# Optimization experiments

Measured on AMD Instinct MI355X. Metric: run time of the kernel, lower is better.

Reference implementation:

```python
import jax, jax.numpy as jnp
import numpy as np

D_MODEL = 1024
N_HEADS = 16
D_HEAD = D_MODEL // N_HEADS
D_FF = 4096
B, L = 4, 2048


def setup_inputs() -> dict:
    key = jax.random.key(0)
    ks = jax.random.split(key, 12)
    s = 0.02
    return {
        "x": jax.random.normal(ks[0], (B, L, D_MODEL), dtype=jnp.float32),
        "ln1_g": jnp.ones((D_MODEL,), jnp.float32),
        "ln1_b": jnp.zeros((D_MODEL,), jnp.float32),
        "w_qkv": jax.random.normal(ks[1], (D_MODEL, 3 * D_MODEL), jnp.float32) * s,
        "b_qkv": jnp.zeros((3 * D_MODEL,), jnp.float32),
        "w_out": jax.random.normal(ks[2], (D_MODEL, D_MODEL), jnp.float32) * s,
        "b_out": jnp.zeros((D_MODEL,), jnp.float32),
        "ln2_g": jnp.ones((D_MODEL,), jnp.float32),
        "ln2_b": jnp.zeros((D_MODEL,), jnp.float32),
        "w1": jax.random.normal(ks[3], (D_MODEL, D_FF), jnp.float32) * s,
        "b1": jnp.zeros((D_FF,), jnp.float32),
        "w2": jax.random.normal(ks[4], (D_FF, D_MODEL), jnp.float32) * s,
        "b2": jnp.zeros((D_MODEL,), jnp.float32),
    }


def _layernorm(x, g, b, eps=1e-5):
    mu = jnp.mean(x, axis=-1, keepdims=True)
    var = jnp.var(x, axis=-1, keepdims=True)
    return (x - mu) * jax.lax.rsqrt(var + eps) * g + b


def _attention(h, w_qkv, b_qkv, w_out, b_out):
    Bx, Lx, D = h.shape
    qkv = h @ w_qkv + b_qkv  # [B,L,3D]
    qkv = qkv.reshape(Bx, Lx, 3, N_HEADS, D_HEAD)
    q, k, v = qkv[:, :, 0], qkv[:, :, 1], qkv[:, :, 2]  # [B,L,H,Dh]
    att = jnp.einsum("bqhd,bkhd->bhqk", q, k) * (D_HEAD ** -0.5)
    causal = jnp.tril(jnp.ones((Lx, Lx), bool))
    att = jnp.where(causal, att, -jnp.inf)
    att = jax.nn.softmax(att, axis=-1)
    out = jnp.einsum("bhqk,bkhd->bqhd", att, v).reshape(Bx, Lx, D)
    return out @ w_out + b_out


def reference(x, ln1_g, ln1_b, w_qkv, b_qkv, w_out, b_out,
              ln2_g, ln2_b, w1, b1, w2, b2):
    h = x + _attention(_layernorm(x, ln1_g, ln1_b), w_qkv, b_qkv, w_out, b_out)
    ff = jax.nn.gelu(_layernorm(h, ln2_g, ln2_b) @ w1 + b1, approximate=False) @ w2 + b2
    return h + ff
```

## Files before the change

### kernel.cpp

```cpp
#include <hip/hip_runtime.h>
#include <hip/hip_bf16.h>


typedef float f32x4 __attribute__((ext_vector_type(4)));
typedef __bf16 bf16x8 __attribute__((ext_vector_type(8)));
typedef unsigned short u16;

#define MFMA16(a, b, c) __builtin_amdgcn_mfma_f32_16x16x32_bf16((a), (b), (c), 0, 0, 0)

#define GLL16(g, l)                                                            \
  __builtin_amdgcn_global_load_lds(                                            \
      (__attribute__((address_space(1))) void*)(g),                            \
      (__attribute__((address_space(3))) void*)(l), 16, 0, 0)

__device__ __forceinline__ u16 f2bf(float f) {
  union { float f; unsigned int u; } x; x.f = f;
  unsigned int r = x.u + 0x7fffu + ((x.u >> 16) & 1u);
  return (u16)(r >> 16);
}

__global__ __launch_bounds__(256) void ln_kernel(
    const float* __restrict__ x, const float* __restrict__ g,
    const float* __restrict__ b, u16* __restrict__ y)
{
  int row = blockIdx.x;
  int t = threadIdx.x;
  const float4* xr = (const float4*)(x + (size_t)row * 1024);
  float4 v = xr[t];
  float s  = v.x + v.y + v.z + v.w;
  float ss = v.x*v.x + v.y*v.y + v.z*v.z + v.w*v.w;
#pragma unroll
  for (int off = 1; off < 64; off <<= 1) {
    s  += __shfl_xor(s, off);
    ss += __shfl_xor(ss, off);
  }
  __shared__ float red[8];
  int w = t >> 6;
  if ((t & 63) == 0) { red[w*2] = s; red[w*2+1] = ss; }
  __syncthreads();
  s  = red[0] + red[2] + red[4] + red[6];
  ss = red[1] + red[3] + red[5] + red[7];
  float mu  = s * (1.0f / 1024.0f);
  float var = ss * (1.0f / 1024.0f) - mu * mu;
  float rs  = rsqrtf(var + 1e-5f);
  float4 gg = ((const float4*)g)[t];
  float4 bb = ((const float4*)b)[t];
  ushort4 o;
  o.x = f2bf((v.x - mu) * rs * gg.x + bb.x);
  o.y = f2bf((v.y - mu) * rs * gg.y + bb.y);
  o.z = f2bf((v.z - mu) * rs * gg.z + bb.z);
  o.w = f2bf((v.w - mu) * rs * gg.w + bb.w);
  ((ushort4*)y)[(size_t)row * 256 + t] = o;
}

__global__ __launch_bounds__(256) void wt_kernel(
    const float* __restrict__ W, u16* __restrict__ Wt, int K, int N)
{
  __shared__ u16 tile[32][33];
  int n0 = blockIdx.x * 32, k0 = blockIdx.y * 32;
  int t = threadIdx.x, tr = t >> 5, tc = t & 31;
#pragma unroll
  for (int i = 0; i < 4; ++i) {
    int k = k0 + tr + i * 8;
    tile[tc][tr + i * 8] = f2bf(W[(size_t)k * N + n0 + tc]);
  }
  __syncthreads();
#pragma unroll
  for (int i = 0; i < 4; ++i) {
    int n = n0 + tr + i * 8;
    Wt[(size_t)n * K + k0 + tc] = tile[tr + i * 8][tc];
  }
}

__global__ __launch_bounds__(256) void vt_kernel(
    const u16* __restrict__ qkv, u16* __restrict__ vt)
{
  __shared__ u16 tile[64][65];
  int bid = blockIdx.x;
  int lt = bid & 31, h = (bid >> 5) & 15, b = bid >> 9;
  int t = threadIdx.x;
  int tr = t >> 4, tc4 = (t & 15) * 4;
  const u16* src = qkv + ((size_t)(b * 2048 + lt * 64)) * 3072 + 2048 + h * 64;
#pragma unroll
  for (int i = 0; i < 4; ++i) {
    int ll = tr + i * 16;
    ushort4 v = *(const ushort4*)(src + (size_t)ll * 3072 + tc4);
    tile[ll][tc4] = v.x; tile[ll][tc4+1] = v.y; tile[ll][tc4+2] = v.z; tile[ll][tc4+3] = v.w;
  }
  __syncthreads();
  u16* dst = vt + ((size_t)(b * 16 + h) * 64) * 2048 + lt * 64;
#pragma unroll
  for (int i = 0; i < 4; ++i) {
    int d = tr + i * 16;
    ushort4 o;
    o.x = tile[tc4][d]; o.y = tile[tc4+1][d]; o.z = tile[tc4+2][d]; o.w = tile[tc4+3][d];
    *(ushort4*)(dst + (size_t)d * 2048 + tc4) = o;
  }
}

template<int BN, int GELU, int HAS_RES, int OUT_BF16>
__global__ __launch_bounds__(512, 2) void gemm_kernel(
    const u16* __restrict__ A, const u16* __restrict__ Bt,
    const float* __restrict__ bias, const float* __restrict__ res,
    void* __restrict__ Cout, int M, int N, int K)
{
  constexpr int WGN = BN / 64;
  constexpr int MW  = (WGN == 4) ? 8 : 4;
  constexpr int LPT = (BN == 256) ? 4 : 3;
  __shared__ u16 lA[4][256 * 32];
  __shared__ u16 lB[4][BN * 32];

  const int nbn = N / BN;
  int nwg = gridDim.x;
  int wg = blockIdx.x;
  if ((nwg & 7) == 0) wg = (wg & 7) * (nwg >> 3) + (wg >> 3);
  int bm = wg / nbn, bn = wg % nbn;
  int tid = threadIdx.x;
  int w = tid >> 6, l = tid & 63;
  int lh = l & 15, lg = l >> 4;
  int wr = w / WGN, wc = w % WGN;
  const size_t Kb = (size_t)K * 2;
  const char* Ab = (const char*)A + (size_t)(bm * 256) * Kb;
  const char* Bb = (const char*)Bt + (size_t)(bn * BN) * Kb;

  const int swst = ((tid ^ (tid >> 3)) & 3) << 4;
  const size_t stR0 = (size_t)(tid >> 2) * Kb + swst;
  const size_t stR1 = stR0 + 128 * Kb;

#define GSTAGE(sel, kt)                                                        \
  do {                                                                         \
    GLL16(Ab + stR0 + (size_t)(kt) * 64, (char*)lA[sel] + tid * 16);           \
    GLL16(Ab + stR1 + (size_t)(kt) * 64, (char*)lA[sel] + tid * 16 + 8192);    \
    GLL16(Bb + stR0 + (size_t)(kt) * 64, (char*)lB[sel] + tid * 16);           \
    if (BN == 256)                                                             \
      GLL16(Bb + stR1 + (size_t)(kt) * 64, (char*)lB[sel] + tid * 16 + 8192);  \
  } while (0)

  const int swo = ((lg ^ (lh >> 1)) & 3) << 4;
  const int offA = (wr * (MW * 16) + lh) * 64 + swo;
  const int offB = (wc * 64 + lh) * 64 + swo;

  f32x4 acc[MW][4] = {};
  const int nkt = K >> 5;
  GSTAGE(0, 0);
  GSTAGE(1, 1);
  GSTAGE(2, 2);
  if (BN == 256) asm volatile("s_waitcnt vmcnt(8)" ::: "memory");
  else           asm volatile("s_waitcnt vmcnt(6)" ::: "memory");
  __builtin_amdgcn_s_barrier();
  __builtin_amdgcn_sched_barrier(0);

#pragma unroll 1
  for (int t = 0; t < nkt; ++t) {
    const char* bufA = (const char*)lA[t & 3];
    const char* bufB = (const char*)lB[t & 3];
    bf16x8 af[MW], bfr[4];
#pragma unroll
    for (int m = 0; m < MW; ++m)
      af[m] = *(const bf16x8*)(bufA + offA + m * 1024);
#pragma unroll
    for (int n = 0; n < 4; ++n)
      bfr[n] = *(const bf16x8*)(bufB + offB + n * 1024);
    if (t + 3 < nkt) GSTAGE((t + 3) & 3, t + 3);
    __builtin_amdgcn_s_setprio(1);
#pragma unroll
    for (int m = 0; m < MW; ++m)
#pragma unroll
      for (int n = 0; n < 4; ++n)
        acc[m][n] = MFMA16(af[m], bfr[n], acc[m][n]);
    __builtin_amdgcn_s_setprio(0);
    if (t < nkt - 1) {
      __builtin_amdgcn_sched_barrier(0);
      if (t < nkt - 3) {
        if (BN == 256) asm volatile("s_waitcnt vmcnt(8)" ::: "memory");
        else           asm volatile("s_waitcnt vmcnt(6)" ::: "memory");
      } else if (t == nkt - 3) {
        if (BN == 256) asm volatile("s_waitcnt vmcnt(4)" ::: "memory");
        else           asm volatile("s_waitcnt vmcnt(3)" ::: "memory");
      } else {
        asm volatile("s_waitcnt vmcnt(0)" ::: "memory");
      }
      __builtin_amdgcn_s_barrier();
      __builtin_amdgcn_sched_barrier(0);
    }
  }
#undef GSTAGE

#pragma unroll
  for (int m = 0; m < MW; ++m) {
    int row0 = bm * 256 + wr * (MW * 16) + m * 16 + lg * 4;
#pragma unroll
    for (int n = 0; n < 4; ++n) {
      int col = bn * BN + wc * 64 + n * 16 + lh;
      float bv = bias[col];
#pragma unroll
      for (int r = 0; r < 4; ++r) {
        int row = row0 + r;
        float v = acc[m][n][r] + bv;
        if (GELU) v = 0.5f * v * (1.0f + erff(v * 0.70710678118f));
        if (HAS_RES) v += res[(size_t)row * N + col];
        if (OUT_BF16) ((u16*)Cout)[(size_t)row * N + col] = f2bf(v);
        else ((float*)Cout)[(size_t)row * N + col] = v;
      }
    }
  }
  (void)M;
}

__global__ __launch_bounds__(256, 4) void attn_kernel(
    const u16* __restrict__ qkv, const u16* __restrict__ vt,
    u16* __restrict__ out)
{
  __shared__ u16 Ks[2][4096];
  __shared__ u16 Vs[2][4096];
  __shared__ u16 Ps[4][1024];

  const float C = 0.18033688011f;

  int bid = blockIdx.x;
  int pi = bid >> 6, bh = bid & 63;
  int b = bh >> 4, h = bh & 15;
  int tid = threadIdx.x;
  int w = tid >> 6, l = tid & 63;
  int lh = l & 15, lg = l >> 4;
  int lh7 = lh & 7;

  const char* kg = (const char*)qkv + (size_t)(b * 2048) * 6144 + 2048 + h * 128;
  const char* vg = (const char*)vt + (size_t)((b * 16 + h) * 64) * 4096;
  char* pbw = (char*)Ps[w] + lh * 128;

#pragma unroll 1
  for (int half = 0; half < 2; ++half) {
    int qb = half ? (31 - pi) : pi;
    int q0 = qb * 64 + w * 16;
    const u16* qbase = qkv + ((size_t)(b * 2048) + q0) * 3072 + h * 64;
    bf16x8 aq0 = *(const bf16x8*)(qbase + (size_t)lh * 3072 + lg * 8);
    bf16x8 aq1 = *(const bf16x8*)(qbase + (size_t)lh * 3072 + 32 + lg * 8);

    f32x4 o[4] = {};
    float m = -1e30f;
    float lsum = 0.f;
    int nt = qb + 1;

    __syncthreads();
#pragma unroll
    for (int i = 0; i < 2; ++i) {
      int u = tid + i * 256;
      int row = u >> 3, uc = u & 7, sw = uc ^ (row & 7);
      GLL16(kg + (size_t)row * 6144 + sw * 16,
            (char*)Ks[0] + (size_t)(i * 256 + w * 64) * 16);
      GLL16(vg + (size_t)row * 4096 + sw * 16,
            (char*)Vs[0] + (size_t)(i * 256 + w * 64) * 16);
    }

#pragma unroll 1
    for (int kt = 0; kt < nt; ++kt) {
      int cur = kt & 1;
      __syncthreads();
      if (kt + 1 < nt) {
        int nxt = cur ^ 1;
        size_t kofs = (size_t)(kt + 1) * 64;
#pragma unroll
        for (int i = 0; i < 2; ++i) {
          int u = tid + i * 256;
          int row = u >> 3, uc = u & 7, sw = uc ^ (row & 7);
          GLL16(kg + (kofs + row) * 6144 + sw * 16,
                (char*)Ks[nxt] + (size_t)(i * 256 + w * 64) * 16);
          GLL16(vg + (size_t)row * 4096 + kofs * 2 + sw * 16,
                (char*)Vs[nxt] + (size_t)(i * 256 + w * 64) * 16);
        }
      }
      const char* kbuf = (const char*)Ks[cur];
      f32x4 s[4];
#pragma unroll
      for (int kb = 0; kb < 4; ++kb) {
        int row = kb * 16 + lh;
        const char* rp = kbuf + row * 128;
        bf16x8 a0 = *(const bf16x8*)(rp + ((lg ^ lh7) << 4));
        bf16x8 a1 = *(const bf16x8*)(rp + (((4 + lg) ^ lh7) << 4));
        f32x4 z = {0.f, 0.f, 0.f, 0.f};
        z = MFMA16(a0, aq0, z);
        z = MFMA16(a1, aq1, z);
        s[kb] = z;
      }
      if (kt == qb) {
        int qin = w * 16 + lh;
#pragma unroll
        for (int kb = 0; kb < 4; ++kb)
#pragma unroll
          for (int r = 0; r < 4; ++r)
            if (kb * 16 + lg * 4 + r > qin) s[kb][r] = -1e30f;
      }
      float tm = fmaxf(fmaxf(s[0][0], s[0][1]), fmaxf(s[0][2], s[0][3]));
#pragma unroll
      for (int kb = 1; kb < 4; ++kb)
        tm = fmaxf(tm, fmaxf(fmaxf(s[kb][0], s[kb][1]), fmaxf(s[kb][2], s[kb][3])));
      tm = fmaxf(tm, __shfl_xor(tm, 16));
      tm = fmaxf(tm, __shfl_xor(tm, 32));
      if (__any(tm > m + 64.0f)) {
        float nm = fmaxf(m, tm);
        float f = __builtin_amdgcn_exp2f((m - nm) * C);
        m = nm; lsum *= f;
#pragma unroll
        for (int db = 0; db < 4; ++db)
#pragma unroll
          for (int r = 0; r < 4; ++r) o[db][r] *= f;
      }
      float mc = m * C;
      float ps = 0.f;
#pragma unroll
      for (int kb = 0; kb < 4; ++kb)
#pragma unroll
        for (int r = 0; r < 4; ++r) {
          float p = __builtin_amdgcn_exp2f(fmaf(s[kb][r], C, -mc));
          s[kb][r] = p;
          ps += p;
        }
      ps += __shfl_xor(ps, 16);
      ps += __shfl_xor(ps, 32);
      lsum += ps;
#pragma unroll
      for (int kb = 0; kb < 4; ++kb) {
        unsigned lo, hi;
        asm("v_cvt_pk_bf16_f32 %0, %1, %2" : "=v"(lo) : "v"(s[kb][0]), "v"(s[kb][1]));
        asm("v_cvt_pk_bf16_f32 %0, %1, %2" : "=v"(hi) : "v"(s[kb][2]), "v"(s[kb][3]));
        int unit = kb * 2 + (lg >> 1);
        uint2 val; val.x = lo; val.y = hi;
        *(uint2*)(pbw + ((unit ^ lh7) << 4) + ((lg & 1) << 3)) = val;
      }
      bf16x8 pa0 = *(const bf16x8*)(pbw + ((lg ^ lh7) << 4));
      bf16x8 pa1 = *(const bf16x8*)(pbw + (((4 + lg) ^ lh7) << 4));
      const char* vbuf = (const char*)Vs[cur];
#pragma unroll
      for (int db = 0; db < 4; ++db) {
        int row = db * 16 + lh;
        const char* rp = vbuf + row * 128;
        bf16x8 v0 = *(const bf16x8*)(rp + ((lg ^ lh7) << 4));
        bf16x8 v1 = *(const bf16x8*)(rp + (((4 + lg) ^ lh7) << 4));
        o[db] = MFMA16(v0, pa0, o[db]);
        o[db] = MFMA16(v1, pa1, o[db]);
      }
    }
    float rinv = 1.0f / lsum;
    u16* ob = out + ((size_t)(b * 2048) + q0 + lh) * 1024 + h * 64;
#pragma unroll
    for (int db = 0; db < 4; ++db) {
      ushort4 pk;
      pk.x = f2bf(o[db][0] * rinv);
      pk.y = f2bf(o[db][1] * rinv);
      pk.z = f2bf(o[db][2] * rinv);
      pk.w = f2bf(o[db][3] * rinv);
      *(ushort4*)(ob + db * 16 + lg * 4) = pk;
    }
  }
}

extern "C" void kernel_launch(void* const* d_in, const int* in_sizes, int n_in,
                              void* d_out, int out_size, void* d_ws, size_t ws_size,
                              hipStream_t stream) {
  const float* x     = (const float*)d_in[0];
  const float* ln1_g = (const float*)d_in[1];
  const float* ln1_b = (const float*)d_in[2];
  const float* w_qkv = (const float*)d_in[3];
  const float* b_qkv = (const float*)d_in[4];
  const float* w_out = (const float*)d_in[5];
  const float* b_out = (const float*)d_in[6];
  const float* ln2_g = (const float*)d_in[7];
  const float* ln2_b = (const float*)d_in[8];
  const float* w1    = (const float*)d_in[9];
  const float* b1    = (const float*)d_in[10];
  const float* w2    = (const float*)d_in[11];
  const float* b2    = (const float*)d_in[12];

  char* ws = (char*)d_ws;
  u16* wqkvT = (u16*)(ws + 0);
  u16* woutT = (u16*)(ws + 6291456);
  u16* w1T   = (u16*)(ws + 8388608);
  u16* w2T   = (u16*)(ws + 16777216);
  u16* qkv   = (u16*)(ws + 25165824);
  u16* ffn1  = (u16*)(ws + 25165824);
  u16* vtb   = (u16*)(ws + 75497472);
  u16* lnb   = (u16*)(ws + 92274688);
  u16* attn  = lnb;
  float* h   = (float*)(ws + 125829120);

  wt_kernel<<<dim3(96, 32), 256, 0, stream>>>(w_qkv, wqkvT, 1024, 3072);
  wt_kernel<<<dim3(32, 32), 256, 0, stream>>>(w_out, woutT, 1024, 1024);
  wt_kernel<<<dim3(128, 32), 256, 0, stream>>>(w1, w1T, 1024, 4096);
  wt_kernel<<<dim3(32, 128), 256, 0, stream>>>(w2, w2T, 4096, 1024);

  ln_kernel<<<8192, 256, 0, stream>>>(x, ln1_g, ln1_b, lnb);
  gemm_kernel<256, 0, 0, 1><<<384, 512, 0, stream>>>(lnb, wqkvT, b_qkv, nullptr, qkv, 8192, 3072, 1024);
  vt_kernel<<<2048, 256, 0, stream>>>(qkv, vtb);
  attn_kernel<<<1024, 256, 0, stream>>>(qkv, vtb, attn);
  gemm_kernel<128, 0, 1, 0><<<256, 512, 0, stream>>>(attn, woutT, b_out, x, h, 8192, 1024, 1024);
  ln_kernel<<<8192, 256, 0, stream>>>(h, ln2_g, ln2_b, lnb);
  gemm_kernel<256, 1, 0, 1><<<512, 512, 0, stream>>>(lnb, w1T, b1, nullptr, ffn1, 8192, 4096, 1024);
  gemm_kernel<128, 0, 1, 0><<<256, 512, 0, stream>>>(ffn1, w2T, b2, h, (float*)d_out, 8192, 1024, 4096);
}
```

Baseline: 398.6 us.

## Switch GEMM to double-buffered pipeline with BK=64 tiles for wide GEMMs

Replaces the 4-stage LDS ring (BK=32) with a 2-stage double buffer, and adds a BK=64 path with an 8-way XOR swizzle for the BN=256 GEMMs. Larger K tiles halve the number of barriers per K, and the 128-wide GEMMs request 4 waves per SIMD for more occupancy. In exchange, only one stage is prefetched ahead, so global latency is less hidden. Each step now ends with a full __syncthreads plus an lgkmcnt(0) wait before the MFMAs, where the old loop used fine-grained vmcnt waits.

```diff
diff --git a/kernel.cpp b/kernel.cpp
--- a/kernel.cpp
+++ b/kernel.cpp
@@ -98,91 +98,113 @@
   }
 }
 
-template<int BN, int GELU, int HAS_RES, int OUT_BF16>
-__global__ __launch_bounds__(512, 2) void gemm_kernel(
+template<int BN, int BK, int GELU, int HAS_RES, int OUT_BF16, int MINW>
+__global__ __launch_bounds__(512, MINW) void gemm_kernel(
     const u16* __restrict__ A, const u16* __restrict__ Bt,
     const float* __restrict__ bias, const float* __restrict__ res,
     void* __restrict__ Cout, int M, int N, int K)
 {
-  constexpr int WGN = BN / 64;
-  constexpr int MW  = (WGN == 4) ? 8 : 4;
-  constexpr int LPT = (BN == 256) ? 4 : 3;
-  __shared__ u16 lA[4][256 * 32];
-  __shared__ u16 lB[4][BN * 32];
+  constexpr int WN = BN / 64;
+  constexpr int MW = (BN == 256) ? 8 : 4;
+  constexpr int RB = BK * 2;
+  __shared__ u16 lA[2][256 * BK];
+  __shared__ u16 lB[2][BN * BK];
 
   const int nbn = N / BN;
   int nwg = gridDim.x;
   int wg = blockIdx.x;
   if ((nwg & 7) == 0) wg = (wg & 7) * (nwg >> 3) + (wg >> 3);
-  int bm = wg / nbn, bn = wg % nbn;
-  int tid = threadIdx.x;
-  int w = tid >> 6, l = tid & 63;
-  int lh = l & 15, lg = l >> 4;
-  int wr = w / WGN, wc = w % WGN;
+  const int bm = wg / nbn, bn = wg % nbn;
+  const int tid = threadIdx.x;
+  const int w = tid >> 6, l = tid & 63;
+  const int lh = l & 15, lg = l >> 4;
+  const int wr = w / WN, wc = w % WN;
   const size_t Kb = (size_t)K * 2;
   const char* Ab = (const char*)A + (size_t)(bm * 256) * Kb;
   const char* Bb = (const char*)Bt + (size_t)(bn * BN) * Kb;
 
-  const int swst = ((tid ^ (tid >> 3)) & 3) << 4;
-  const size_t stR0 = (size_t)(tid >> 2) * Kb + swst;
-  const size_t stR1 = stR0 + 128 * Kb;
+  const int jsrc = (BK == 64)
+      ? (((tid & 7) ^ ((tid >> 3) & 7)) << 4)
+      : (((tid ^ (tid >> 3)) & 3) << 4);
 
 #define GSTAGE(sel, kt)                                                        \
   do {                                                                         \
-    GLL16(Ab + stR0 + (size_t)(kt) * 64, (char*)lA[sel] + tid * 16);           \
-    GLL16(Ab + stR1 + (size_t)(kt) * 64, (char*)lA[sel] + tid * 16 + 8192);    \
-    GLL16(Bb + stR0 + (size_t)(kt) * 64, (char*)lB[sel] + tid * 16);           \
-    if (BN == 256)                                                             \
-      GLL16(Bb + stR1 + (size_t)(kt) * 64, (char*)lB[sel] + tid * 16 + 8192);  \
+    if (BK == 64) {                                                            \
+      const char* as = Ab + (size_t)(tid >> 3) * Kb + (size_t)(kt) * 128 + jsrc;\
+      const char* bs = Bb + (size_t)(tid >> 3) * Kb + (size_t)(kt) * 128 + jsrc;\
+      char* ad = (char*)lA[sel] + tid * 16;                                    \
+      char* bd = (char*)lB[sel] + tid * 16;                                    \
+      GLL16(as, ad);                 GLL16(as + 64 * Kb, ad + 8192);           \
+      GLL16(as + 128 * Kb, ad + 16384); GLL16(as + 192 * Kb, ad + 24576);     \
+      GLL16(bs, bd);                 GLL16(bs + 64 * Kb, bd + 8192);           \
+      GLL16(bs + 128 * Kb, bd + 16384); GLL16(bs + 192 * Kb, bd + 24576);     \
+    } else {                                                                   \
+      const char* as = Ab + (size_t)(tid >> 2) * Kb + (size_t)(kt) * 64 + jsrc;\
+      char* ad = (char*)lA[sel] + tid * 16;                                    \
+      GLL16(as, ad); GLL16(as + 128 * Kb, ad + 8192);                          \
+      GLL16(Bb + (size_t)(tid >> 2) * Kb + (size_t)(kt) * 64 + jsrc,           \
+            (char*)lB[sel] + tid * 16);                                        \
+    }                                                                          \
   } while (0)
 
-  const int swo = ((lg ^ (lh >> 1)) & 3) << 4;
-  const int offA = (wr * (MW * 16) + lh) * 64 + swo;
-  const int offB = (wc * 64 + lh) * 64 + swo;
+  const int rowA = wr * (MW * 16) + lh;
+  const int rowB = wc * 64 + lh;
+  const int x640 = ((lg ^ (lh & 7)) & 7) << 4;
+  const int x641 = (((4 + lg) ^ (lh & 7)) & 7) << 4;
+  const int x32  = ((lg ^ (lh >> 1)) & 3) << 4;
+  const int offA0 = rowA * RB + ((BK == 64) ? x640 : x32);
+  const int offA1 = rowA * RB + ((BK == 64) ? x641 : 0);
+  const int offB0 = rowB * RB + ((BK == 64) ? x640 : x32);
+  const int offB1 = rowB * RB + ((BK == 64) ? x641 : 0);
 
   f32x4 acc[MW][4] = {};
-  const int nkt = K >> 5;
+  const int nkt = K / BK;
   GSTAGE(0, 0);
-  GSTAGE(1, 1);
-  GSTAGE(2, 2);
-  if (BN == 256) asm volatile("s_waitcnt vmcnt(8)" ::: "memory");
-  else           asm volatile("s_waitcnt vmcnt(6)" ::: "memory");
-  __builtin_amdgcn_s_barrier();
-  __builtin_amdgcn_sched_barrier(0);
-
+  __syncthreads();
 #pragma unroll 1
   for (int t = 0; t < nkt; ++t) {
-    const char* bufA = (const char*)lA[t & 3];
-    const char* bufB = (const char*)lB[t & 3];
-    bf16x8 af[MW], bfr[4];
-#pragma unroll
-    for (int m = 0; m < MW; ++m)
-      af[m] = *(const bf16x8*)(bufA + offA + m * 1024);
-#pragma unroll
-    for (int n = 0; n < 4; ++n)
-      bfr[n] = *(const bf16x8*)(bufB + offB + n * 1024);
-    if (t + 3 < nkt) GSTAGE((t + 3) & 3, t + 3);
-    __builtin_amdgcn_s_setprio(1);
-#pragma unroll
-    for (int m = 0; m < MW; ++m)
+    const int cur = t & 1;
+    if (t + 1 < nkt) GSTAGE(cur ^ 1, t + 1);
+    __builtin_amdgcn_sched_barrier(0);
+    const char* bufA = (const char*)lA[cur];
+    const char* bufB = (const char*)lB[cur];
+    {
+      bf16x8 af[MW], bfr[4];
+#pragma unroll
+      for (int m = 0; m < MW; ++m)
+        af[m] = *(const bf16x8*)(bufA + offA0 + m * 16 * RB);
 #pragma unroll
       for (int n = 0; n < 4; ++n)
-        acc[m][n] = MFMA16(af[m], bfr[n], acc[m][n]);
-    __builtin_amdgcn_s_setprio(0);
-    if (t < nkt - 1) {
+        bfr[n] = *(const bf16x8*)(bufB + offB0 + n * 16 * RB);
+      asm volatile("s_waitcnt lgkmcnt(0)" ::: "memory");
       __builtin_amdgcn_sched_barrier(0);
-      if (t < nkt - 3) {
-        if (BN == 256) asm volatile("s_waitcnt vmcnt(8)" ::: "memory");
-        else           asm volatile("s_waitcnt vmcnt(6)" ::: "memory");
-      } else if (t == nkt - 3) {
-        if (BN == 256) asm volatile("s_waitcnt vmcnt(4)" ::: "memory");
-        else           asm volatile("s_waitcnt vmcnt(3)" ::: "memory");
-      } else {
-        asm volatile("s_waitcnt vmcnt(0)" ::: "memory");
-      }
-      __builtin_amdgcn_s_barrier();
+      __builtin_amdgcn_s_setprio(1);
+#pragma unroll
+      for (int m = 0; m < MW; ++m)
+#pragma unroll
+        for (int n = 0; n < 4; ++n)
+          acc[m][n] = MFMA16(af[m], bfr[n], acc[m][n]);
+      __builtin_amdgcn_s_setprio(0);
+    }
+    if (BK == 64) {
+      bf16x8 af[MW], bfr[4];
+#pragma unroll
+      for (int m = 0; m < MW; ++m)
+        af[m] = *(const bf16x8*)(bufA + offA1 + m * 16 * RB);
+#pragma unroll
+      for (int n = 0; n < 4; ++n)
+        bfr[n] = *(const bf16x8*)(bufB + offB1 + n * 16 * RB);
+      asm volatile("s_waitcnt lgkmcnt(0)" ::: "memory");
       __builtin_amdgcn_sched_barrier(0);
-    }
+      __builtin_amdgcn_s_setprio(1);
+#pragma unroll
+      for (int m = 0; m < MW; ++m)
+#pragma unroll
+        for (int n = 0; n < 4; ++n)
+          acc[m][n] = MFMA16(af[m], bfr[n], acc[m][n]);
+      __builtin_amdgcn_s_setprio(0);
+    }
+    __syncthreads();
   }
 #undef GSTAGE
 
@@ -390,11 +412,11 @@
   wt_kernel<<<dim3(32, 128), 256, 0, stream>>>(w2, w2T, 4096, 1024);
 
   ln_kernel<<<8192, 256, 0, stream>>>(x, ln1_g, ln1_b, lnb);
-  gemm_kernel<256, 0, 0, 1><<<384, 512, 0, stream>>>(lnb, wqkvT, b_qkv, nullptr, qkv, 8192, 3072, 1024);
+  gemm_kernel<256, 64, 0, 0, 1, 2><<<384, 512, 0, stream>>>(lnb, wqkvT, b_qkv, nullptr, qkv, 8192, 3072, 1024);
   vt_kernel<<<2048, 256, 0, stream>>>(qkv, vtb);
   attn_kernel<<<1024, 256, 0, stream>>>(qkv, vtb, attn);
-  gemm_kernel<128, 0, 1, 0><<<256, 512, 0, stream>>>(attn, woutT, b_out, x, h, 8192, 1024, 1024);
+  gemm_kernel<128, 32, 0, 1, 0, 4><<<256, 512, 0, stream>>>(attn, woutT, b_out, x, h, 8192, 1024, 1024);
   ln_kernel<<<8192, 256, 0, stream>>>(h, ln2_g, ln2_b, lnb);
-  gemm_kernel<256, 1, 0, 1><<<512, 512, 0, stream>>>(lnb, w1T, b1, nullptr, ffn1, 8192, 4096, 1024);
-  gemm_kernel<128, 0, 1, 0><<<256, 512, 0, stream>>>(ffn1, w2T, b2, h, (float*)d_out, 8192, 1024, 4096);
-}
+  gemm_kernel<256, 64, 1, 0, 1, 2><<<512, 512, 0, stream>>>(lnb, w1T, b1, nullptr, ffn1, 8192, 4096, 1024);
+  gemm_kernel<128, 32, 0, 1, 0, 4><<<256, 512, 0, stream>>>(ffn1, w2T, b2, h, (float*)d_out, 8192, 1024, 4096);
+}
```

New measurement: 438.0 us. 9.9% more time.
